# Kernel tuning notes

Measured on AMD Instinct MI355X. Metric: run time of the kernel, lower is better.

## Reference

```python
import jax, jax.numpy as jnp
import numpy as np

B, T, U, H = 4, 256, 64, 512
INNER, VOCAB = 512, 1024


def setup_inputs() -> dict:
    key = jax.random.key(0)
    ks = jax.random.split(key, 6)
    s_in = 1.0 / np.sqrt(2 * H)
    s_h = 1.0 / np.sqrt(INNER)
    return {
        "enc_state": jax.random.normal(ks[0], (B, T, H), dtype=jnp.float32),
        "dec_state": jax.random.normal(ks[1], (B, U, H), dtype=jnp.float32),
        "W1": jax.random.normal(ks[2], (2 * H, INNER), dtype=jnp.float32) * s_in,
        "b1": jnp.zeros((INNER,), dtype=jnp.float32),
        "W2": jax.random.normal(ks[3], (INNER, VOCAB), dtype=jnp.float32) * s_h,
        "b2": jnp.zeros((VOCAB,), dtype=jnp.float32),
    }


def reference(enc_state, dec_state, W1, b1, W2, b2):
    # JointNet: broadcast enc [B,T,1,H] and dec [B,1,U,H], concat -> Linear -> tanh -> Linear -> log_softmax
    # concat+Linear is split into two smaller matmuls (mathematically identical):
    # cat([e,d]) @ W1 == e @ W1[:H] + d @ W1[H:]
    enc_proj = jnp.einsum("bth,hi->bti", enc_state, W1[:H])      # [B,T,INNER]
    dec_proj = jnp.einsum("buh,hi->bui", dec_state, W1[H:])      # [B,U,INNER]
    hidden = jnp.tanh(enc_proj[:, :, None, :] + dec_proj[:, None, :, :] + b1)  # [B,T,U,INNER]
    logits = jnp.einsum("btui,iv->btuv", hidden, W2) + b2        # [B,T,U,VOCAB]
    return jax.nn.log_softmax(logits, axis=-1)
```

## Files before the change

### kernel.cpp

```cpp
#include <hip/hip_runtime.h>
#include <hip/hip_bf16.h>
#include <cstdint>
#include <cstddef>


typedef __attribute__((ext_vector_type(8))) short short8;
typedef __attribute__((ext_vector_type(4))) float f32x4;

#define BS_CHUNK 65536

#define WS_EP_OFF 0
#define WS_DP_OFF (1024 * 512 * 4)
#define WS_W2_OFF (WS_DP_OFF + 256 * 512 * 4)

#define SMEM_TOTAL (65536 + 4096 + 256 + 4096 + 256)

__device__ __forceinline__ unsigned short f2bf(float x) {
  unsigned int u = __builtin_bit_cast(unsigned int, x);
  u += 0x7FFFu + ((u >> 16) & 1u);
  return (unsigned short)(u >> 16);
}

__device__ __forceinline__ float fast_tanh(float x) {
  float ax = fabsf(x);
  float e = __expf(-2.0f * ax);
  float t = (1.0f - e) * __builtin_amdgcn_rcpf(1.0f + e);
  return copysignf(t, x);
}

__global__ __launch_bounds__(512) void prep(
    const float* __restrict__ enc, const float* __restrict__ dec,
    const float* __restrict__ W1, const float* __restrict__ b1,
    const float* __restrict__ W2,
    float* __restrict__ ep, float* __restrict__ dp, char* __restrict__ w2st) {
  __shared__ float As[8 * 512];
  const int tid = threadIdx.x;
  if (blockIdx.x < 160) {
    const int r0 = blockIdx.x * 8;
    const bool isenc = (r0 < 1024);
    const float* A = isenc ? (enc + (size_t)r0 * 512) : (dec + (size_t)(r0 - 1024) * 512);
    const float* W = isenc ? W1 : (W1 + 512 * 512);
    float* O = isenc ? (ep + (size_t)r0 * 512) : (dp + (size_t)(r0 - 1024) * 512);

    for (int idx = tid; idx < 8 * 512; idx += 512) As[idx] = A[idx];
    __syncthreads();

    const int c = tid;
    float acc[8];
#pragma unroll
    for (int r = 0; r < 8; ++r) acc[r] = 0.0f;
    const float4* As4 = (const float4*)As;
#pragma unroll 2
    for (int k4 = 0; k4 < 128; ++k4) {
      const int kb = k4 * 4;
      float w0 = W[(size_t)(kb + 0) * 512 + c];
      float w1 = W[(size_t)(kb + 1) * 512 + c];
      float w2 = W[(size_t)(kb + 2) * 512 + c];
      float w3 = W[(size_t)(kb + 3) * 512 + c];
#pragma unroll
      for (int r = 0; r < 8; ++r) {
        float4 a = As4[r * 128 + k4];
        acc[r] += a.x * w0 + a.y * w1 + a.z * w2 + a.w * w3;
      }
    }
    const float bias = isenc ? b1[c] : 0.0f;
#pragma unroll
    for (int r = 0; r < 8; ++r) O[(size_t)r * 512 + c] = acc[r] + bias;
  } else {
    const int g = (blockIdx.x - 160) * 512 + tid;
    const int v = g & 1023;
    const int kc = g >> 10;
    unsigned short vals[32];
#pragma unroll
    for (int ki = 0; ki < 32; ++ki)
      vals[ki] = f2bf(W2[(size_t)(kc * 32 + ki) * 1024 + v]);
    uint4* dst = (uint4*)(w2st + (size_t)kc * BS_CHUNK + (size_t)v * 64);
    const uint4* s = (const uint4*)vals;
    dst[0] = s[0]; dst[1] = s[1]; dst[2] = s[2]; dst[3] = s[3];
  }
}

__global__ __launch_bounds__(1024, 4) void joint(
    const float* __restrict__ ep, const float* __restrict__ dp,
    const char* __restrict__ w2st, const float* __restrict__ b2,
    float* __restrict__ out) {
  extern __shared__ char smem[];
  char* As = smem;
  float* redM = (float*)(smem + 65536);
  float* redF = redM + 1024;
  float* redS = redF + 64;
  float* redF2 = redS + 1024;

  const int tid = threadIdx.x;
  const int wave = tid >> 6, lane = tid & 63;
  const int lo = lane & 15, hi = lane >> 4;
  const int bt = blockIdx.x;
  const int m0 = bt * 64;
  const int dprow0 = (bt >> 8) * 64;
  const int nbase = wave * 64;
  const int krot = bt & 15;

  const char* bbase = w2st + (size_t)(nbase + lo) * 64 + hi * 16;

  short8 b[4];
  {
    const char* src = bbase + (size_t)krot * BS_CHUNK;
#pragma unroll
    for (int ni = 0; ni < 4; ++ni) b[ni] = *(const short8*)(src + ni * 1024);
  }

  {
    const int c0 = (tid & 63) * 8;
    const int rg = tid >> 6;
    const float* epr = ep + (size_t)bt * 512 + c0;
    float e0[8];
    *(float4*)(e0) = *(const float4*)(epr);
    *(float4*)(e0 + 4) = *(const float4*)(epr + 4);
#pragma unroll
    for (int p = 0; p < 4; ++p) {
      const int row = rg + p * 16;
      const float* dpr = dp + (size_t)(dprow0 + row) * 512 + c0;
      float d0[8];
      *(float4*)(d0) = *(const float4*)(dpr);
      *(float4*)(d0 + 4) = *(const float4*)(dpr + 4);
      unsigned short h[8];
#pragma unroll
      for (int j = 0; j < 8; ++j) h[j] = f2bf(fast_tanh(e0[j] + d0[j]));
      *(uint4*)(As + ((row * 1024 + c0 * 2) ^ ((row & 7) << 4))) = *(const uint4*)h;
    }
  }

  f32x4 acc[4][4];
#pragma unroll
  for (int mi = 0; mi < 4; ++mi)
#pragma unroll
    for (int ni = 0; ni < 4; ++ni)
#pragma unroll
      for (int j = 0; j < 4; ++j) acc[mi][ni][j] = 0.0f;

  __syncthreads();

#pragma unroll 1
  for (int kc = 0; kc < 16; ++kc) {
    int kci = kc + krot;
    kci = (kci >= 16) ? kci - 16 : kci;
    short8 bn[4];
    if (kc < 15) {
      int kn = kci + 1;
      kn = (kn >= 16) ? 0 : kn;
      const char* src = bbase + (size_t)kn * BS_CHUNK;
#pragma unroll
      for (int ni = 0; ni < 4; ++ni) bn[ni] = *(const short8*)(src + ni * 1024);
    }
    short8 a[4];
#pragma unroll
    for (int mi = 0; mi < 4; ++mi) {
      const int row = mi * 16 + lo;
      a[mi] = *(const short8*)(As + ((row * 1024 + kci * 64 + hi * 16) ^ ((row & 7) << 4)));
    }
    __builtin_amdgcn_s_setprio(1);
#pragma unroll
    for (int ni = 0; ni < 4; ++ni)
#pragma unroll
      for (int mi = 0; mi < 4; ++mi)
        acc[mi][ni] = __builtin_amdgcn_mfma_f32_16x16x32_bf16(a[mi], b[ni], acc[mi][ni], 0, 0, 0);
    __builtin_amdgcn_s_setprio(0);
    if (kc < 15) {
#pragma unroll
      for (int ni = 0; ni < 4; ++ni) b[ni] = bn[ni];
    }
  }

  float b2v[4];
#pragma unroll
  for (int ni = 0; ni < 4; ++ni) b2v[ni] = b2[nbase + ni * 16 + lo];
#pragma unroll
  for (int mi = 0; mi < 4; ++mi)
#pragma unroll
    for (int ni = 0; ni < 4; ++ni)
#pragma unroll
      for (int j = 0; j < 4; ++j) acc[mi][ni][j] += b2v[ni];

  float pm[4][4];
#pragma unroll
  for (int mi = 0; mi < 4; ++mi)
#pragma unroll
    for (int r = 0; r < 4; ++r) {
      float m = fmaxf(fmaxf(acc[mi][0][r], acc[mi][1][r]),
                      fmaxf(acc[mi][2][r], acc[mi][3][r]));
      pm[mi][r] = m;
    }
#pragma unroll
  for (int off = 1; off < 16; off <<= 1)
#pragma unroll
    for (int mi = 0; mi < 4; ++mi)
#pragma unroll
      for (int r = 0; r < 4; ++r)
        pm[mi][r] = fmaxf(pm[mi][r], __shfl_xor(pm[mi][r], off));
  if (lo == 0) {
#pragma unroll
    for (int mi = 0; mi < 4; ++mi)
#pragma unroll
      for (int r = 0; r < 4; ++r)
        redM[wave * 64 + mi * 16 + hi * 4 + r] = pm[mi][r];
  }
  __syncthreads();
  {
    const int tr = tid >> 4, w = tid & 15;
    float v = redM[w * 64 + tr];
#pragma unroll
    for (int off = 1; off < 16; off <<= 1) v = fmaxf(v, __shfl_xor(v, off));
    if (w == 0) redF[tr] = v;
  }
  __syncthreads();
  float rm[4][4];
#pragma unroll
  for (int mi = 0; mi < 4; ++mi)
#pragma unroll
    for (int r = 0; r < 4; ++r) rm[mi][r] = redF[mi * 16 + hi * 4 + r];

  float ps[4][4];
#pragma unroll
  for (int mi = 0; mi < 4; ++mi)
#pragma unroll
    for (int r = 0; r < 4; ++r) {
      float s = 0.0f;
#pragma unroll
      for (int ni = 0; ni < 4; ++ni) s += __expf(acc[mi][ni][r] - rm[mi][r]);
      ps[mi][r] = s;
    }
#pragma unroll
  for (int off = 1; off < 16; off <<= 1)
#pragma unroll
    for (int mi = 0; mi < 4; ++mi)
#pragma unroll
      for (int r = 0; r < 4; ++r)
        ps[mi][r] += __shfl_xor(ps[mi][r], off);
  if (lo == 0) {
#pragma unroll
    for (int mi = 0; mi < 4; ++mi)
#pragma unroll
      for (int r = 0; r < 4; ++r)
        redS[wave * 64 + mi * 16 + hi * 4 + r] = ps[mi][r];
  }
  __syncthreads();
  {
    const int tr = tid >> 4, w = tid & 15;
    float v = redS[w * 64 + tr];
#pragma unroll
    for (int off = 1; off < 16; off <<= 1) v += __shfl_xor(v, off);
    if (w == 0) redF2[tr] = v;
  }
  __syncthreads();

#pragma unroll
  for (int mi = 0; mi < 4; ++mi)
#pragma unroll
    for (int r = 0; r < 4; ++r) {
      const int row = mi * 16 + hi * 4 + r;
      const float sub = rm[mi][r] + __logf(redF2[row]);
      float* op = out + (size_t)(m0 + row) * 1024 + nbase + lo;
#pragma unroll
      for (int ni = 0; ni < 4; ++ni) op[ni * 16] = acc[mi][ni][r] - sub;
    }
}

extern "C" void kernel_launch(void* const* d_in, const int* in_sizes, int n_in,
                              void* d_out, int out_size, void* d_ws, size_t ws_size,
                              hipStream_t stream) {
  const float* enc = (const float*)d_in[0];
  const float* dec = (const float*)d_in[1];
  const float* W1  = (const float*)d_in[2];
  const float* b1  = (const float*)d_in[3];
  const float* W2  = (const float*)d_in[4];
  const float* b2  = (const float*)d_in[5];
  float* out = (float*)d_out;

  char* ws = (char*)d_ws;
  float* ep = (float*)(ws + WS_EP_OFF);
  float* dp = (float*)(ws + WS_DP_OFF);
  char* w2st = ws + WS_W2_OFF;

  prep<<<192, 512, 0, stream>>>(enc, dec, W1, b1, W2, ep, dp, w2st);
  joint<<<1024, 1024, SMEM_TOTAL, stream>>>(ep, dp, w2st, b2, out);
}
```

Baseline: 190.3 us.

## Make joint kernel process four row tiles per block with double-buffered W2 prefetch

The joint kernel now launches 256 blocks instead of 1024, and each block loops over four consecutive 64-row tiles. W2 fragments are kept in two register sets (P/Q) that are prefetched two K-chunks ahead, and the next tile's first chunks are loaded during the softmax epilogue. The bias load is hoisted out of the tile loop. __syncthreads is replaced by a barrier macro that only waits on LDS counters, and the setprio hints are removed. The aim is to hide global-load latency and amortise per-block setup, at the cost of fewer resident blocks per CU, so tanh/store phases may overlap less with MFMA work from other blocks.

```diff
diff --git a/kernel.cpp b/kernel.cpp
--- a/kernel.cpp
+++ b/kernel.cpp
@@ -14,6 +14,13 @@
 #define WS_W2_OFF (WS_DP_OFF + 256 * 512 * 4)
 
 #define SMEM_TOTAL (65536 + 4096 + 256 + 4096 + 256)
+
+#define BAR()                                                   \
+  do {                                                          \
+    asm volatile("s_waitcnt lgkmcnt(0)" ::: "memory");          \
+    __builtin_amdgcn_s_barrier();                               \
+    __builtin_amdgcn_sched_barrier(0);                          \
+  } while (0)
 
 __device__ __forceinline__ unsigned short f2bf(float x) {
   unsigned int u = __builtin_bit_cast(unsigned int, x);
@@ -94,175 +101,203 @@
   const int tid = threadIdx.x;
   const int wave = tid >> 6, lane = tid & 63;
   const int lo = lane & 15, hi = lane >> 4;
-  const int bt = blockIdx.x;
-  const int m0 = bt * 64;
-  const int dprow0 = (bt >> 8) * 64;
   const int nbase = wave * 64;
-  const int krot = bt & 15;
-
   const char* bbase = w2st + (size_t)(nbase + lo) * 64 + hi * 16;
 
-  short8 b[4];
+  float b2v[4];
+#pragma unroll
+  for (int ni = 0; ni < 4; ++ni) b2v[ni] = b2[nbase + ni * 16 + lo];
+
+  short8 P[4], Q[4];
   {
-    const char* src = bbase + (size_t)krot * BS_CHUNK;
-#pragma unroll
-    for (int ni = 0; ni < 4; ++ni) b[ni] = *(const short8*)(src + ni * 1024);
+    const int bt0 = blockIdx.x * 4;
+    const int kr = bt0 & 15;
+    const char* s0 = bbase + (size_t)kr * BS_CHUNK;
+    const char* s1 = bbase + (size_t)((kr + 1) & 15) * BS_CHUNK;
+#pragma unroll
+    for (int ni = 0; ni < 4; ++ni) P[ni] = *(const short8*)(s0 + ni * 1024);
+#pragma unroll
+    for (int ni = 0; ni < 4; ++ni) Q[ni] = *(const short8*)(s1 + ni * 1024);
   }
 
-  {
-    const int c0 = (tid & 63) * 8;
-    const int rg = tid >> 6;
-    const float* epr = ep + (size_t)bt * 512 + c0;
-    float e0[8];
-    *(float4*)(e0) = *(const float4*)(epr);
-    *(float4*)(e0 + 4) = *(const float4*)(epr + 4);
-#pragma unroll
-    for (int p = 0; p < 4; ++p) {
-      const int row = rg + p * 16;
-      const float* dpr = dp + (size_t)(dprow0 + row) * 512 + c0;
-      float d0[8];
-      *(float4*)(d0) = *(const float4*)(dpr);
-      *(float4*)(d0 + 4) = *(const float4*)(dpr + 4);
-      unsigned short h[8];
-#pragma unroll
-      for (int j = 0; j < 8; ++j) h[j] = f2bf(fast_tanh(e0[j] + d0[j]));
-      *(uint4*)(As + ((row * 1024 + c0 * 2) ^ ((row & 7) << 4))) = *(const uint4*)h;
-    }
+#pragma unroll 1
+  for (int t = 0; t < 4; ++t) {
+    const int bt = blockIdx.x * 4 + t;
+    const int m0 = bt * 64;
+    const int dprow0 = (bt >> 8) * 64;
+    const int krot = bt & 15;
+
+    {
+      const int c0 = (tid & 63) * 8;
+      const int rg = tid >> 6;
+      const float* epr = ep + (size_t)bt * 512 + c0;
+      float e0[8];
+      *(float4*)(e0) = *(const float4*)(epr);
+      *(float4*)(e0 + 4) = *(const float4*)(epr + 4);
+#pragma unroll
+      for (int p = 0; p < 4; ++p) {
+        const int row = rg + p * 16;
+        const float* dpr = dp + (size_t)(dprow0 + row) * 512 + c0;
+        float d0[8];
+        *(float4*)(d0) = *(const float4*)(dpr);
+        *(float4*)(d0 + 4) = *(const float4*)(dpr + 4);
+        unsigned short h[8];
+#pragma unroll
+        for (int j = 0; j < 8; ++j) h[j] = f2bf(fast_tanh(e0[j] + d0[j]));
+        *(uint4*)(As + ((row * 1024 + c0 * 2) ^ ((row & 7) << 4))) = *(const uint4*)h;
+      }
+    }
+
+    f32x4 acc[4][4];
+#pragma unroll
+    for (int mi = 0; mi < 4; ++mi)
+#pragma unroll
+      for (int ni = 0; ni < 4; ++ni)
+#pragma unroll
+        for (int j = 0; j < 4; ++j) acc[mi][ni][j] = 0.0f;
+
+    BAR();
+
+#pragma unroll 1
+    for (int i = 0; i < 8; ++i) {
+      const int c0 = (2 * i + krot) & 15;
+      const int c1 = (c0 + 1) & 15;
+      {
+        short8 a[4];
+#pragma unroll
+        for (int mi = 0; mi < 4; ++mi) {
+          const int row = mi * 16 + lo;
+          a[mi] = *(const short8*)(As + ((row * 1024 + c0 * 64 + hi * 16) ^ ((row & 7) << 4)));
+        }
+#pragma unroll
+        for (int ni = 0; ni < 4; ++ni)
+#pragma unroll
+          for (int mi = 0; mi < 4; ++mi)
+            acc[mi][ni] = __builtin_amdgcn_mfma_f32_16x16x32_bf16(a[mi], P[ni], acc[mi][ni], 0, 0, 0);
+      }
+      if (i < 7) {
+        const char* src = bbase + (size_t)((c0 + 2) & 15) * BS_CHUNK;
+#pragma unroll
+        for (int ni = 0; ni < 4; ++ni) P[ni] = *(const short8*)(src + ni * 1024);
+      }
+      {
+        short8 a[4];
+#pragma unroll
+        for (int mi = 0; mi < 4; ++mi) {
+          const int row = mi * 16 + lo;
+          a[mi] = *(const short8*)(As + ((row * 1024 + c1 * 64 + hi * 16) ^ ((row & 7) << 4)));
+        }
+#pragma unroll
+        for (int ni = 0; ni < 4; ++ni)
+#pragma unroll
+          for (int mi = 0; mi < 4; ++mi)
+            acc[mi][ni] = __builtin_amdgcn_mfma_f32_16x16x32_bf16(a[mi], Q[ni], acc[mi][ni], 0, 0, 0);
+      }
+      if (i < 7) {
+        const char* src = bbase + (size_t)((c1 + 2) & 15) * BS_CHUNK;
+#pragma unroll
+        for (int ni = 0; ni < 4; ++ni) Q[ni] = *(const short8*)(src + ni * 1024);
+      }
+    }
+
+#pragma unroll
+    for (int mi = 0; mi < 4; ++mi)
+#pragma unroll
+      for (int ni = 0; ni < 4; ++ni)
+#pragma unroll
+        for (int j = 0; j < 4; ++j) acc[mi][ni][j] += b2v[ni];
+
+    float pm[4][4];
+#pragma unroll
+    for (int mi = 0; mi < 4; ++mi)
+#pragma unroll
+      for (int r = 0; r < 4; ++r)
+        pm[mi][r] = fmaxf(fmaxf(acc[mi][0][r], acc[mi][1][r]),
+                          fmaxf(acc[mi][2][r], acc[mi][3][r]));
+#pragma unroll
+    for (int off = 1; off < 16; off <<= 1)
+#pragma unroll
+      for (int mi = 0; mi < 4; ++mi)
+#pragma unroll
+        for (int r = 0; r < 4; ++r)
+          pm[mi][r] = fmaxf(pm[mi][r], __shfl_xor(pm[mi][r], off));
+    if (lo == 0) {
+#pragma unroll
+      for (int mi = 0; mi < 4; ++mi)
+#pragma unroll
+        for (int r = 0; r < 4; ++r)
+          redM[wave * 64 + mi * 16 + hi * 4 + r] = pm[mi][r];
+    }
+    BAR();
+    {
+      const int tr = tid >> 4, w = tid & 15;
+      float v = redM[w * 64 + tr];
+#pragma unroll
+      for (int off = 1; off < 16; off <<= 1) v = fmaxf(v, __shfl_xor(v, off));
+      if (w == 0) redF[tr] = v;
+    }
+    BAR();
+    float rm[4][4];
+#pragma unroll
+    for (int mi = 0; mi < 4; ++mi)
+#pragma unroll
+      for (int r = 0; r < 4; ++r) rm[mi][r] = redF[mi * 16 + hi * 4 + r];
+
+    float ps[4][4];
+#pragma unroll
+    for (int mi = 0; mi < 4; ++mi)
+#pragma unroll
+      for (int r = 0; r < 4; ++r) {
+        float s = 0.0f;
+#pragma unroll
+        for (int ni = 0; ni < 4; ++ni) s += __expf(acc[mi][ni][r] - rm[mi][r]);
+        ps[mi][r] = s;
+      }
+#pragma unroll
+    for (int off = 1; off < 16; off <<= 1)
+#pragma unroll
+      for (int mi = 0; mi < 4; ++mi)
+#pragma unroll
+        for (int r = 0; r < 4; ++r)
+          ps[mi][r] += __shfl_xor(ps[mi][r], off);
+    if (lo == 0) {
+#pragma unroll
+      for (int mi = 0; mi < 4; ++mi)
+#pragma unroll
+        for (int r = 0; r < 4; ++r)
+          redS[wave * 64 + mi * 16 + hi * 4 + r] = ps[mi][r];
+    }
+    BAR();
+    {
+      const int tr = tid >> 4, w = tid & 15;
+      float v = redS[w * 64 + tr];
+#pragma unroll
+      for (int off = 1; off < 16; off <<= 1) v += __shfl_xor(v, off);
+      if (w == 0) redF2[tr] = v;
+    }
+    BAR();
+
+    if (t < 3) {
+      const int nrot = (bt + 1) & 15;
+      const char* s0 = bbase + (size_t)nrot * BS_CHUNK;
+      const char* s1 = bbase + (size_t)((nrot + 1) & 15) * BS_CHUNK;
+#pragma unroll
+      for (int ni = 0; ni < 4; ++ni) P[ni] = *(const short8*)(s0 + ni * 1024);
+#pragma unroll
+      for (int ni = 0; ni < 4; ++ni) Q[ni] = *(const short8*)(s1 + ni * 1024);
+    }
+
+#pragma unroll
+    for (int mi = 0; mi < 4; ++mi)
+#pragma unroll
+      for (int r = 0; r < 4; ++r) {
+        const int row = mi * 16 + hi * 4 + r;
+        const float sub = rm[mi][r] + __logf(redF2[row]);
+        float* op = out + (size_t)(m0 + row) * 1024 + nbase + lo;
+#pragma unroll
+        for (int ni = 0; ni < 4; ++ni) op[ni * 16] = acc[mi][ni][r] - sub;
+      }
   }
-
-  f32x4 acc[4][4];
-#pragma unroll
-  for (int mi = 0; mi < 4; ++mi)
-#pragma unroll
-    for (int ni = 0; ni < 4; ++ni)
-#pragma unroll
-      for (int j = 0; j < 4; ++j) acc[mi][ni][j] = 0.0f;
-
-  __syncthreads();
-
-#pragma unroll 1
-  for (int kc = 0; kc < 16; ++kc) {
-    int kci = kc + krot;
-    kci = (kci >= 16) ? kci - 16 : kci;
-    short8 bn[4];
-    if (kc < 15) {
-      int kn = kci + 1;
-      kn = (kn >= 16) ? 0 : kn;
-      const char* src = bbase + (size_t)kn * BS_CHUNK;
-#pragma unroll
-      for (int ni = 0; ni < 4; ++ni) bn[ni] = *(const short8*)(src + ni * 1024);
-    }
-    short8 a[4];
-#pragma unroll
-    for (int mi = 0; mi < 4; ++mi) {
-      const int row = mi * 16 + lo;
-      a[mi] = *(const short8*)(As + ((row * 1024 + kci * 64 + hi * 16) ^ ((row & 7) << 4)));
-    }
-    __builtin_amdgcn_s_setprio(1);
-#pragma unroll
-    for (int ni = 0; ni < 4; ++ni)
-#pragma unroll
-      for (int mi = 0; mi < 4; ++mi)
-        acc[mi][ni] = __builtin_amdgcn_mfma_f32_16x16x32_bf16(a[mi], b[ni], acc[mi][ni], 0, 0, 0);
-    __builtin_amdgcn_s_setprio(0);
-    if (kc < 15) {
-#pragma unroll
-      for (int ni = 0; ni < 4; ++ni) b[ni] = bn[ni];
-    }
-  }
-
-  float b2v[4];
-#pragma unroll
-  for (int ni = 0; ni < 4; ++ni) b2v[ni] = b2[nbase + ni * 16 + lo];
-#pragma unroll
-  for (int mi = 0; mi < 4; ++mi)
-#pragma unroll
-    for (int ni = 0; ni < 4; ++ni)
-#pragma unroll
-      for (int j = 0; j < 4; ++j) acc[mi][ni][j] += b2v[ni];
-
-  float pm[4][4];
-#pragma unroll
-  for (int mi = 0; mi < 4; ++mi)
-#pragma unroll
-    for (int r = 0; r < 4; ++r) {
-      float m = fmaxf(fmaxf(acc[mi][0][r], acc[mi][1][r]),
-                      fmaxf(acc[mi][2][r], acc[mi][3][r]));
-      pm[mi][r] = m;
-    }
-#pragma unroll
-  for (int off = 1; off < 16; off <<= 1)
-#pragma unroll
-    for (int mi = 0; mi < 4; ++mi)
-#pragma unroll
-      for (int r = 0; r < 4; ++r)
-        pm[mi][r] = fmaxf(pm[mi][r], __shfl_xor(pm[mi][r], off));
-  if (lo == 0) {
-#pragma unroll
-    for (int mi = 0; mi < 4; ++mi)
-#pragma unroll
-      for (int r = 0; r < 4; ++r)
-        redM[wave * 64 + mi * 16 + hi * 4 + r] = pm[mi][r];
-  }
-  __syncthreads();
-  {
-    const int tr = tid >> 4, w = tid & 15;
-    float v = redM[w * 64 + tr];
-#pragma unroll
-    for (int off = 1; off < 16; off <<= 1) v = fmaxf(v, __shfl_xor(v, off));
-    if (w == 0) redF[tr] = v;
-  }
-  __syncthreads();
-  float rm[4][4];
-#pragma unroll
-  for (int mi = 0; mi < 4; ++mi)
-#pragma unroll
-    for (int r = 0; r < 4; ++r) rm[mi][r] = redF[mi * 16 + hi * 4 + r];
-
-  float ps[4][4];
-#pragma unroll
-  for (int mi = 0; mi < 4; ++mi)
-#pragma unroll
-    for (int r = 0; r < 4; ++r) {
-      float s = 0.0f;
-#pragma unroll
-      for (int ni = 0; ni < 4; ++ni) s += __expf(acc[mi][ni][r] - rm[mi][r]);
-      ps[mi][r] = s;
-    }
-#pragma unroll
-  for (int off = 1; off < 16; off <<= 1)
-#pragma unroll
-    for (int mi = 0; mi < 4; ++mi)
-#pragma unroll
-      for (int r = 0; r < 4; ++r)
-        ps[mi][r] += __shfl_xor(ps[mi][r], off);
-  if (lo == 0) {
-#pragma unroll
-    for (int mi = 0; mi < 4; ++mi)
-#pragma unroll
-      for (int r = 0; r < 4; ++r)
-        redS[wave * 64 + mi * 16 + hi * 4 + r] = ps[mi][r];
-  }
-  __syncthreads();
-  {
-    const int tr = tid >> 4, w = tid & 15;
-    float v = redS[w * 64 + tr];
-#pragma unroll
-    for (int off = 1; off < 16; off <<= 1) v += __shfl_xor(v, off);
-    if (w == 0) redF2[tr] = v;
-  }
-  __syncthreads();
-
-#pragma unroll
-  for (int mi = 0; mi < 4; ++mi)
-#pragma unroll
-    for (int r = 0; r < 4; ++r) {
-      const int row = mi * 16 + hi * 4 + r;
-      const float sub = rm[mi][r] + __logf(redF2[row]);
-      float* op = out + (size_t)(m0 + row) * 1024 + nbase + lo;
-#pragma unroll
-      for (int ni = 0; ni < 4; ++ni) op[ni * 16] = acc[mi][ni][r] - sub;
-    }
 }
 
 extern "C" void kernel_launch(void* const* d_in, const int* in_sizes, int n_in,
@@ -282,5 +317,5 @@
   char* w2st = ws + WS_W2_OFF;
 
   prep<<<192, 512, 0, stream>>>(enc, dec, W1, b1, W2, ep, dp, w2st);
-  joint<<<1024, 1024, SMEM_TOTAL, stream>>>(ep, dp, w2st, b2, out);
-}
+  joint<<<256, 1024, SMEM_TOTAL, stream>>>(ep, dp, w2st, b2, out);
+}
```

Result: slower. 308.0 us (+61.9%).

## Stage W2 chunks into LDS with async double buffering and per-quarter A tiles

Applied to the files above, without the earlier changes.

The joint kernel now stages W2 K-chunks into LDS with global_load_lds, double-buffered, instead of having each wave load its B fragments straight from global memory. The tanh/bf16 activation tile is built one 128-column quarter at a time in a 16KB region, so it overlaps with the chunk loads. __syncthreads is replaced by explicit waitcnt plus s_barrier. The prep kernel's projection is split into 4-row blocks to launch more blocks. The shared-memory footprint grows to 144KB, which likely limits the kernel to one 1024-thread block per CU and trades occupancy for explicit overlap.

```diff
diff --git a/kernel.cpp b/kernel.cpp
--- a/kernel.cpp
+++ b/kernel.cpp
@@ -13,7 +13,9 @@
 #define WS_DP_OFF (1024 * 512 * 4)
 #define WS_W2_OFF (WS_DP_OFF + 256 * 512 * 4)
 
-#define SMEM_TOTAL (65536 + 4096 + 256 + 4096 + 256)
+#define LDS_B0 16384
+#define LDS_B1 81920
+#define SMEM_TOTAL 147456
 
 __device__ __forceinline__ unsigned short f2bf(float x) {
   unsigned int u = __builtin_bit_cast(unsigned int, x);
@@ -33,24 +35,22 @@
     const float* __restrict__ W1, const float* __restrict__ b1,
     const float* __restrict__ W2,
     float* __restrict__ ep, float* __restrict__ dp, char* __restrict__ w2st) {
-  __shared__ float As[8 * 512];
+  __shared__ float As[4 * 512];
   const int tid = threadIdx.x;
-  if (blockIdx.x < 160) {
-    const int r0 = blockIdx.x * 8;
+  if (blockIdx.x < 320) {
+    const int r0 = blockIdx.x * 4;
     const bool isenc = (r0 < 1024);
     const float* A = isenc ? (enc + (size_t)r0 * 512) : (dec + (size_t)(r0 - 1024) * 512);
     const float* W = isenc ? W1 : (W1 + 512 * 512);
     float* O = isenc ? (ep + (size_t)r0 * 512) : (dp + (size_t)(r0 - 1024) * 512);
 
-    for (int idx = tid; idx < 8 * 512; idx += 512) As[idx] = A[idx];
+    for (int idx = tid; idx < 4 * 512; idx += 512) As[idx] = A[idx];
     __syncthreads();
 
     const int c = tid;
-    float acc[8];
-#pragma unroll
-    for (int r = 0; r < 8; ++r) acc[r] = 0.0f;
+    float acc[4] = {0.f, 0.f, 0.f, 0.f};
     const float4* As4 = (const float4*)As;
-#pragma unroll 2
+#pragma unroll 4
     for (int k4 = 0; k4 < 128; ++k4) {
       const int kb = k4 * 4;
       float w0 = W[(size_t)(kb + 0) * 512 + c];
@@ -58,16 +58,16 @@
       float w2 = W[(size_t)(kb + 2) * 512 + c];
       float w3 = W[(size_t)(kb + 3) * 512 + c];
 #pragma unroll
-      for (int r = 0; r < 8; ++r) {
+      for (int r = 0; r < 4; ++r) {
         float4 a = As4[r * 128 + k4];
         acc[r] += a.x * w0 + a.y * w1 + a.z * w2 + a.w * w3;
       }
     }
     const float bias = isenc ? b1[c] : 0.0f;
 #pragma unroll
-    for (int r = 0; r < 8; ++r) O[(size_t)r * 512 + c] = acc[r] + bias;
+    for (int r = 0; r < 4; ++r) O[(size_t)r * 512 + c] = acc[r] + bias;
   } else {
-    const int g = (blockIdx.x - 160) * 512 + tid;
+    const int g = (blockIdx.x - 320) * 512 + tid;
     const int v = g & 1023;
     const int kc = g >> 10;
     unsigned short vals[32];
@@ -80,13 +80,24 @@
   }
 }
 
+__device__ __forceinline__ void stage_chunk(const char* __restrict__ w2st,
+                                            char* dstbuf, int gc, int wave, int lane) {
+  const char* src = w2st + (size_t)gc * BS_CHUNK + wave * 4096 + (size_t)lane * 16;
+  char* dst = dstbuf + wave * 4096 + lane * 16;
+#pragma unroll
+  for (int jj = 0; jj < 4; ++jj)
+    __builtin_amdgcn_global_load_lds(
+        (const __attribute__((address_space(1))) unsigned int*)(src + jj * 1024),
+        (__attribute__((address_space(3))) unsigned int*)(dst + jj * 1024), 16, 0, 0);
+}
+
 __global__ __launch_bounds__(1024, 4) void joint(
     const float* __restrict__ ep, const float* __restrict__ dp,
     const char* __restrict__ w2st, const float* __restrict__ b2,
     float* __restrict__ out) {
   extern __shared__ char smem[];
-  char* As = smem;
-  float* redM = (float*)(smem + 65536);
+  char* Asm = smem;
+  float* redM = (float*)smem;
   float* redF = redM + 1024;
   float* redS = redF + 64;
   float* redF2 = redS + 1024;
@@ -98,98 +109,109 @@
   const int m0 = bt * 64;
   const int dprow0 = (bt >> 8) * 64;
   const int nbase = wave * 64;
-  const int krot = bt & 15;
-
-  const char* bbase = w2st + (size_t)(nbase + lo) * 64 + hi * 16;
-
-  short8 b[4];
+  const int krot4 = bt & 3;
+
+  const int tr = tid >> 4;
+  const int tc = (tid & 15) * 8;
+
+  float b2v[4];
+#pragma unroll
+  for (int ni = 0; ni < 4; ++ni) b2v[ni] = b2[nbase + ni * 16 + lo];
+
+  float e0[8], d0[8];
   {
-    const char* src = bbase + (size_t)krot * BS_CHUNK;
-#pragma unroll
-    for (int ni = 0; ni < 4; ++ni) b[ni] = *(const short8*)(src + ni * 1024);
-  }
-
+    const float* epr = ep + (size_t)bt * 512 + tc;
+    *(float4*)(e0) = ((const float4*)epr)[0];
+    *(float4*)(e0 + 4) = ((const float4*)epr)[1];
+    const float* dpr = dp + (size_t)(dprow0 + tr) * 512 + tc;
+    *(float4*)(d0) = ((const float4*)dpr)[0];
+    *(float4*)(d0 + 4) = ((const float4*)dpr)[1];
+  }
+  stage_chunk(w2st, smem + LDS_B0, (0 + krot4) & 3, wave, lane);
+  stage_chunk(w2st, smem + LDS_B1, (1 + krot4) & 3, wave, lane);
+  __builtin_amdgcn_sched_barrier(0);
   {
-    const int c0 = (tid & 63) * 8;
-    const int rg = tid >> 6;
-    const float* epr = ep + (size_t)bt * 512 + c0;
-    float e0[8];
-    *(float4*)(e0) = *(const float4*)(epr);
-    *(float4*)(e0 + 4) = *(const float4*)(epr + 4);
-#pragma unroll
-    for (int p = 0; p < 4; ++p) {
-      const int row = rg + p * 16;
-      const float* dpr = dp + (size_t)(dprow0 + row) * 512 + c0;
-      float d0[8];
-      *(float4*)(d0) = *(const float4*)(dpr);
-      *(float4*)(d0 + 4) = *(const float4*)(dpr + 4);
+    unsigned short h[8];
+#pragma unroll
+    for (int j = 0; j < 8; ++j) h[j] = f2bf(fast_tanh(e0[j] + d0[j]));
+    *(uint4*)(Asm + ((tr * 256 + tc * 2) ^ ((tr & 7) << 4))) = *(const uint4*)h;
+  }
+
+  f32x4 acc[4][4];
+#pragma unroll
+  for (int mi = 0; mi < 4; ++mi)
+#pragma unroll
+    for (int ni = 0; ni < 4; ++ni)
+#pragma unroll
+      for (int j = 0; j < 4; ++j) acc[mi][ni][j] = 0.0f;
+
+#pragma unroll
+  for (int q = 0; q < 4; ++q) {
+    if (q) {
+      const float* epr = ep + (size_t)bt * 512 + q * 128 + tc;
+      float e1[8], d1[8];
+      *(float4*)(e1) = ((const float4*)epr)[0];
+      *(float4*)(e1 + 4) = ((const float4*)epr)[1];
+      const float* dpr = dp + (size_t)(dprow0 + tr) * 512 + q * 128 + tc;
+      *(float4*)(d1) = ((const float4*)dpr)[0];
+      *(float4*)(d1 + 4) = ((const float4*)dpr)[1];
       unsigned short h[8];
 #pragma unroll
-      for (int j = 0; j < 8; ++j) h[j] = f2bf(fast_tanh(e0[j] + d0[j]));
-      *(uint4*)(As + ((row * 1024 + c0 * 2) ^ ((row & 7) << 4))) = *(const uint4*)h;
-    }
-  }
-
-  f32x4 acc[4][4];
+      for (int j = 0; j < 8; ++j) h[j] = f2bf(fast_tanh(e1[j] + d1[j]));
+      *(uint4*)(Asm + ((tr * 256 + tc * 2) ^ ((tr & 7) << 4))) = *(const uint4*)h;
+    }
+#pragma unroll
+    for (int ii = 0; ii < 4; ++ii) {
+      const int i = q * 4 + ii;
+      if (i == 15) asm volatile("s_waitcnt vmcnt(0) lgkmcnt(0)" ::: "memory");
+      else         asm volatile("s_waitcnt vmcnt(4) lgkmcnt(0)" ::: "memory");
+      __builtin_amdgcn_s_barrier();
+      __builtin_amdgcn_sched_barrier(0);
+
+      char* rdbuf = smem + ((i & 1) ? LDS_B1 : LDS_B0);
+      const int cif = (i + krot4) & 3;
+      short8 bfr[4], afr[4];
+      const char* bp = rdbuf + (size_t)(nbase + lo) * 64 + hi * 16;
+#pragma unroll
+      for (int ni = 0; ni < 4; ++ni) bfr[ni] = *(const short8*)(bp + ni * 1024);
+#pragma unroll
+      for (int mi = 0; mi < 4; ++mi) {
+        const int row = mi * 16 + lo;
+        afr[mi] = *(const short8*)(Asm + ((row * 256 + cif * 64 + hi * 16) ^ ((row & 7) << 4)));
+      }
+      asm volatile("s_waitcnt lgkmcnt(0)" ::: "memory");
+      __builtin_amdgcn_sched_barrier(0);
+      __builtin_amdgcn_s_barrier();
+      __builtin_amdgcn_sched_barrier(0);
+
+      if (i < 14) {
+        const int j = i + 2;
+        const int gc = (j >> 2) * 4 + ((j + krot4) & 3);
+        stage_chunk(w2st, rdbuf, gc, wave, lane);
+        __builtin_amdgcn_sched_barrier(0);
+      }
+#pragma unroll
+      for (int ni = 0; ni < 4; ++ni)
+#pragma unroll
+        for (int mi = 0; mi < 4; ++mi)
+          acc[mi][ni] = __builtin_amdgcn_mfma_f32_16x16x32_bf16(afr[mi], bfr[ni], acc[mi][ni], 0, 0, 0);
+    }
+  }
+
 #pragma unroll
   for (int mi = 0; mi < 4; ++mi)
 #pragma unroll
     for (int ni = 0; ni < 4; ++ni)
 #pragma unroll
-      for (int j = 0; j < 4; ++j) acc[mi][ni][j] = 0.0f;
-
-  __syncthreads();
-
-#pragma unroll 1
-  for (int kc = 0; kc < 16; ++kc) {
-    int kci = kc + krot;
-    kci = (kci >= 16) ? kci - 16 : kci;
-    short8 bn[4];
-    if (kc < 15) {
-      int kn = kci + 1;
-      kn = (kn >= 16) ? 0 : kn;
-      const char* src = bbase + (size_t)kn * BS_CHUNK;
-#pragma unroll
-      for (int ni = 0; ni < 4; ++ni) bn[ni] = *(const short8*)(src + ni * 1024);
-    }
-    short8 a[4];
-#pragma unroll
-    for (int mi = 0; mi < 4; ++mi) {
-      const int row = mi * 16 + lo;
-      a[mi] = *(const short8*)(As + ((row * 1024 + kci * 64 + hi * 16) ^ ((row & 7) << 4)));
-    }
-    __builtin_amdgcn_s_setprio(1);
-#pragma unroll
-    for (int ni = 0; ni < 4; ++ni)
-#pragma unroll
-      for (int mi = 0; mi < 4; ++mi)
-        acc[mi][ni] = __builtin_amdgcn_mfma_f32_16x16x32_bf16(a[mi], b[ni], acc[mi][ni], 0, 0, 0);
-    __builtin_amdgcn_s_setprio(0);
-    if (kc < 15) {
-#pragma unroll
-      for (int ni = 0; ni < 4; ++ni) b[ni] = bn[ni];
-    }
-  }
-
-  float b2v[4];
-#pragma unroll
-  for (int ni = 0; ni < 4; ++ni) b2v[ni] = b2[nbase + ni * 16 + lo];
-#pragma unroll
-  for (int mi = 0; mi < 4; ++mi)
-#pragma unroll
-    for (int ni = 0; ni < 4; ++ni)
-#pragma unroll
       for (int j = 0; j < 4; ++j) acc[mi][ni][j] += b2v[ni];
 
   float pm[4][4];
 #pragma unroll
   for (int mi = 0; mi < 4; ++mi)
 #pragma unroll
-    for (int r = 0; r < 4; ++r) {
-      float m = fmaxf(fmaxf(acc[mi][0][r], acc[mi][1][r]),
-                      fmaxf(acc[mi][2][r], acc[mi][3][r]));
-      pm[mi][r] = m;
-    }
+    for (int r = 0; r < 4; ++r)
+      pm[mi][r] = fmaxf(fmaxf(acc[mi][0][r], acc[mi][1][r]),
+                        fmaxf(acc[mi][2][r], acc[mi][3][r]));
 #pragma unroll
   for (int off = 1; off < 16; off <<= 1)
 #pragma unroll
@@ -204,15 +226,17 @@
       for (int r = 0; r < 4; ++r)
         redM[wave * 64 + mi * 16 + hi * 4 + r] = pm[mi][r];
   }
-  __syncthreads();
+  asm volatile("s_waitcnt lgkmcnt(0)" ::: "memory");
+  __builtin_amdgcn_s_barrier();
   {
-    const int tr = tid >> 4, w = tid & 15;
-    float v = redM[w * 64 + tr];
+    const int rr = tid >> 4, w = tid & 15;
+    float v = redM[w * 64 + rr];
 #pragma unroll
     for (int off = 1; off < 16; off <<= 1) v = fmaxf(v, __shfl_xor(v, off));
-    if (w == 0) redF[tr] = v;
-  }
-  __syncthreads();
+    if (w == 0) redF[rr] = v;
+  }
+  asm volatile("s_waitcnt lgkmcnt(0)" ::: "memory");
+  __builtin_amdgcn_s_barrier();
   float rm[4][4];
 #pragma unroll
   for (int mi = 0; mi < 4; ++mi)
@@ -243,15 +267,17 @@
       for (int r = 0; r < 4; ++r)
         redS[wave * 64 + mi * 16 + hi * 4 + r] = ps[mi][r];
   }
-  __syncthreads();
+  asm volatile("s_waitcnt lgkmcnt(0)" ::: "memory");
+  __builtin_amdgcn_s_barrier();
   {
-    const int tr = tid >> 4, w = tid & 15;
-    float v = redS[w * 64 + tr];
+    const int rr = tid >> 4, w = tid & 15;
+    float v = redS[w * 64 + rr];
 #pragma unroll
     for (int off = 1; off < 16; off <<= 1) v += __shfl_xor(v, off);
-    if (w == 0) redF2[tr] = v;
-  }
-  __syncthreads();
+    if (w == 0) redF2[rr] = v;
+  }
+  asm volatile("s_waitcnt lgkmcnt(0)" ::: "memory");
+  __builtin_amdgcn_s_barrier();
 
 #pragma unroll
   for (int mi = 0; mi < 4; ++mi)
@@ -281,6 +307,6 @@
   float* dp = (float*)(ws + WS_DP_OFF);
   char* w2st = ws + WS_W2_OFF;
 
-  prep<<<192, 512, 0, stream>>>(enc, dec, W1, b1, W2, ep, dp, w2st);
+  prep<<<352, 512, 0, stream>>>(enc, dec, W1, b1, W2, ep, dp, w2st);
   joint<<<1024, 1024, SMEM_TOTAL, stream>>>(ep, dp, w2st, b2, out);
 }
```

New measurement: 257.5 us. 35.3% more time.

## Split joint kernel into tiled GEMM with fp16 logits plus separate log-softmax pass

Applied to the files above, without the earlier changes.

Replaces the fused GEMM+log_softmax kernel with two kernels. The first is a 256x256-tiled GEMM that recomputes tanh(enc+dec) per k-chunk into double-buffered LDS and writes bias-added logits as fp16 into the output buffer. The second is a per-row log-softmax kernel that reads those fp16 values back and overwrites the row in place with fp32 results. The intent is to free the GEMM from the block-wide softmax reductions and their barriers. In exchange it adds an extra write and read of the full logits, repeats the tanh work across the four N blocks, rounds logits to fp16, and drops the max subtraction, which risks overflow and accuracy loss.

```diff
diff --git a/kernel.cpp b/kernel.cpp
--- a/kernel.cpp
+++ b/kernel.cpp
@@ -13,12 +13,19 @@
 #define WS_DP_OFF (1024 * 512 * 4)
 #define WS_W2_OFF (WS_DP_OFF + 256 * 512 * 4)
 
-#define SMEM_TOTAL (65536 + 4096 + 256 + 4096 + 256)
-
 __device__ __forceinline__ unsigned short f2bf(float x) {
   unsigned int u = __builtin_bit_cast(unsigned int, x);
   u += 0x7FFFu + ((u >> 16) & 1u);
   return (unsigned short)(u >> 16);
+}
+
+__device__ __forceinline__ unsigned short f2h(float x) {
+  _Float16 h = (_Float16)x;
+  return __builtin_bit_cast(unsigned short, h);
+}
+
+__device__ __forceinline__ float h2f(unsigned short u) {
+  return (float)__builtin_bit_cast(_Float16, u);
 }
 
 __device__ __forceinline__ float fast_tanh(float x) {
@@ -80,54 +87,41 @@
   }
 }
 
-__global__ __launch_bounds__(1024, 4) void joint(
+__global__ __launch_bounds__(1024, 4) void joint_gemm(
     const float* __restrict__ ep, const float* __restrict__ dp,
     const char* __restrict__ w2st, const float* __restrict__ b2,
     float* __restrict__ out) {
-  extern __shared__ char smem[];
-  char* As = smem;
-  float* redM = (float*)(smem + 65536);
-  float* redF = redM + 1024;
-  float* redS = redF + 64;
-  float* redF2 = redS + 1024;
+  __shared__ char As[2][256 * 64];
 
   const int tid = threadIdx.x;
   const int wave = tid >> 6, lane = tid & 63;
   const int lo = lane & 15, hi = lane >> 4;
-  const int bt = blockIdx.x;
-  const int m0 = bt * 64;
-  const int dprow0 = (bt >> 8) * 64;
-  const int nbase = wave * 64;
-  const int krot = bt & 15;
+  const int wm = wave >> 2, wn = wave & 3;
+  const int m = blockIdx.x & 255, n = blockIdx.x >> 8;
+  const int row0 = m * 256;
+  const int nbase = n * 256 + wn * 64;
+
+  const int tr = tid >> 2;
+  const int ts = tid & 3;
+  const int grow = row0 + tr;
+  const int gbt = grow >> 6;
+  const int gdr = ((gbt >> 8) << 6) + (grow & 63);
+  const float* eprow = ep + (size_t)gbt * 512 + ts * 8;
+  const float* dprow = dp + (size_t)gdr * 512 + ts * 8;
+  const int wofs = tr * 64 + ((ts ^ ((tr >> 1) & 3)) << 4);
 
   const char* bbase = w2st + (size_t)(nbase + lo) * 64 + hi * 16;
 
-  short8 b[4];
   {
-    const char* src = bbase + (size_t)krot * BS_CHUNK;
-#pragma unroll
-    for (int ni = 0; ni < 4; ++ni) b[ni] = *(const short8*)(src + ni * 1024);
-  }
-
-  {
-    const int c0 = (tid & 63) * 8;
-    const int rg = tid >> 6;
-    const float* epr = ep + (size_t)bt * 512 + c0;
-    float e0[8];
-    *(float4*)(e0) = *(const float4*)(epr);
-    *(float4*)(e0 + 4) = *(const float4*)(epr + 4);
-#pragma unroll
-    for (int p = 0; p < 4; ++p) {
-      const int row = rg + p * 16;
-      const float* dpr = dp + (size_t)(dprow0 + row) * 512 + c0;
-      float d0[8];
-      *(float4*)(d0) = *(const float4*)(dpr);
-      *(float4*)(d0 + 4) = *(const float4*)(dpr + 4);
-      unsigned short h[8];
-#pragma unroll
-      for (int j = 0; j < 8; ++j) h[j] = f2bf(fast_tanh(e0[j] + d0[j]));
-      *(uint4*)(As + ((row * 1024 + c0 * 2) ^ ((row & 7) << 4))) = *(const uint4*)h;
-    }
+    float e[8], d[8];
+    *(float4*)(e) = *(const float4*)(eprow);
+    *(float4*)(e + 4) = *(const float4*)(eprow + 4);
+    *(float4*)(d) = *(const float4*)(dprow);
+    *(float4*)(d + 4) = *(const float4*)(dprow + 4);
+    unsigned short h[8];
+#pragma unroll
+    for (int j = 0; j < 8; ++j) h[j] = f2bf(fast_tanh(e[j] + d[j]));
+    *(uint4*)(As[0] + wofs) = *(const uint4*)h;
   }
 
   f32x4 acc[4][4];
@@ -142,127 +136,86 @@
 
 #pragma unroll 1
   for (int kc = 0; kc < 16; ++kc) {
-    int kci = kc + krot;
-    kci = (kci >= 16) ? kci - 16 : kci;
-    short8 bn[4];
+    short8 b[4];
+    const char* bp = bbase + (size_t)kc * BS_CHUNK;
+#pragma unroll
+    for (int ni = 0; ni < 4; ++ni) b[ni] = *(const short8*)(bp + ni * 1024);
+
     if (kc < 15) {
-      int kn = kci + 1;
-      kn = (kn >= 16) ? 0 : kn;
-      const char* src = bbase + (size_t)kn * BS_CHUNK;
-#pragma unroll
-      for (int ni = 0; ni < 4; ++ni) bn[ni] = *(const short8*)(src + ni * 1024);
-    }
+      float e[8], d[8];
+      const float* e_ = eprow + (kc + 1) * 32;
+      const float* d_ = dprow + (kc + 1) * 32;
+      *(float4*)(e) = *(const float4*)(e_);
+      *(float4*)(e + 4) = *(const float4*)(e_ + 4);
+      *(float4*)(d) = *(const float4*)(d_);
+      *(float4*)(d + 4) = *(const float4*)(d_ + 4);
+      unsigned short h[8];
+#pragma unroll
+      for (int j = 0; j < 8; ++j) h[j] = f2bf(fast_tanh(e[j] + d[j]));
+      *(uint4*)(As[(kc + 1) & 1] + wofs) = *(const uint4*)h;
+    }
+
     short8 a[4];
 #pragma unroll
     for (int mi = 0; mi < 4; ++mi) {
-      const int row = mi * 16 + lo;
-      a[mi] = *(const short8*)(As + ((row * 1024 + kci * 64 + hi * 16) ^ ((row & 7) << 4)));
-    }
-    __builtin_amdgcn_s_setprio(1);
+      const int r = wm * 64 + mi * 16 + lo;
+      a[mi] = *(const short8*)(As[kc & 1] + r * 64 + ((hi ^ ((r >> 1) & 3)) << 4));
+    }
 #pragma unroll
     for (int ni = 0; ni < 4; ++ni)
 #pragma unroll
       for (int mi = 0; mi < 4; ++mi)
         acc[mi][ni] = __builtin_amdgcn_mfma_f32_16x16x32_bf16(a[mi], b[ni], acc[mi][ni], 0, 0, 0);
-    __builtin_amdgcn_s_setprio(0);
-    if (kc < 15) {
-#pragma unroll
-      for (int ni = 0; ni < 4; ++ni) b[ni] = bn[ni];
-    }
+
+    __syncthreads();
   }
 
   float b2v[4];
 #pragma unroll
   for (int ni = 0; ni < 4; ++ni) b2v[ni] = b2[nbase + ni * 16 + lo];
+
+  unsigned short* outh = (unsigned short*)out;
 #pragma unroll
   for (int mi = 0; mi < 4; ++mi)
 #pragma unroll
-    for (int ni = 0; ni < 4; ++ni)
-#pragma unroll
-      for (int j = 0; j < 4; ++j) acc[mi][ni][j] += b2v[ni];
-
-  float pm[4][4];
-#pragma unroll
-  for (int mi = 0; mi < 4; ++mi)
-#pragma unroll
     for (int r = 0; r < 4; ++r) {
-      float m = fmaxf(fmaxf(acc[mi][0][r], acc[mi][1][r]),
-                      fmaxf(acc[mi][2][r], acc[mi][3][r]));
-      pm[mi][r] = m;
-    }
-#pragma unroll
-  for (int off = 1; off < 16; off <<= 1)
-#pragma unroll
-    for (int mi = 0; mi < 4; ++mi)
-#pragma unroll
-      for (int r = 0; r < 4; ++r)
-        pm[mi][r] = fmaxf(pm[mi][r], __shfl_xor(pm[mi][r], off));
-  if (lo == 0) {
-#pragma unroll
-    for (int mi = 0; mi < 4; ++mi)
-#pragma unroll
-      for (int r = 0; r < 4; ++r)
-        redM[wave * 64 + mi * 16 + hi * 4 + r] = pm[mi][r];
-  }
-  __syncthreads();
-  {
-    const int tr = tid >> 4, w = tid & 15;
-    float v = redM[w * 64 + tr];
-#pragma unroll
-    for (int off = 1; off < 16; off <<= 1) v = fmaxf(v, __shfl_xor(v, off));
-    if (w == 0) redF[tr] = v;
-  }
-  __syncthreads();
-  float rm[4][4];
-#pragma unroll
-  for (int mi = 0; mi < 4; ++mi)
-#pragma unroll
-    for (int r = 0; r < 4; ++r) rm[mi][r] = redF[mi * 16 + hi * 4 + r];
-
-  float ps[4][4];
-#pragma unroll
-  for (int mi = 0; mi < 4; ++mi)
-#pragma unroll
-    for (int r = 0; r < 4; ++r) {
-      float s = 0.0f;
-#pragma unroll
-      for (int ni = 0; ni < 4; ++ni) s += __expf(acc[mi][ni][r] - rm[mi][r]);
-      ps[mi][r] = s;
-    }
-#pragma unroll
-  for (int off = 1; off < 16; off <<= 1)
-#pragma unroll
-    for (int mi = 0; mi < 4; ++mi)
-#pragma unroll
-      for (int r = 0; r < 4; ++r)
-        ps[mi][r] += __shfl_xor(ps[mi][r], off);
-  if (lo == 0) {
-#pragma unroll
-    for (int mi = 0; mi < 4; ++mi)
-#pragma unroll
-      for (int r = 0; r < 4; ++r)
-        redS[wave * 64 + mi * 16 + hi * 4 + r] = ps[mi][r];
-  }
-  __syncthreads();
-  {
-    const int tr = tid >> 4, w = tid & 15;
-    float v = redS[w * 64 + tr];
-#pragma unroll
-    for (int off = 1; off < 16; off <<= 1) v += __shfl_xor(v, off);
-    if (w == 0) redF2[tr] = v;
-  }
-  __syncthreads();
-
-#pragma unroll
-  for (int mi = 0; mi < 4; ++mi)
-#pragma unroll
-    for (int r = 0; r < 4; ++r) {
-      const int row = mi * 16 + hi * 4 + r;
-      const float sub = rm[mi][r] + __logf(redF2[row]);
-      float* op = out + (size_t)(m0 + row) * 1024 + nbase + lo;
-#pragma unroll
-      for (int ni = 0; ni < 4; ++ni) op[ni * 16] = acc[mi][ni][r] - sub;
-    }
+      const int row = row0 + wm * 64 + mi * 16 + hi * 4 + r;
+      unsigned short* op = outh + (size_t)row * 2048 + nbase + lo;
+#pragma unroll
+      for (int ni = 0; ni < 4; ++ni)
+        op[ni * 16] = f2h(acc[mi][ni][r] + b2v[ni]);
+    }
+}
+
+__global__ __launch_bounds__(256) void lsm(float* __restrict__ out) {
+  const int gw = (blockIdx.x * 256 + threadIdx.x) >> 6;
+  const int lane = threadIdx.x & 63;
+#pragma unroll 1
+  for (int r = gw; r < 65536; r += 8192) {
+    const unsigned short* lp = (const unsigned short*)out + (size_t)r * 2048 + lane * 16;
+    uint4 q0 = *(const uint4*)(lp);
+    uint4 q1 = *(const uint4*)(lp + 8);
+    unsigned short us[16];
+    *(uint4*)(us) = q0;
+    *(uint4*)(us + 8) = q1;
+    float v[16];
+#pragma unroll
+    for (int j = 0; j < 16; ++j) v[j] = h2f(us[j]);
+    float s = 0.0f;
+#pragma unroll
+    for (int j = 0; j < 16; ++j) s += __expf(v[j]);
+#pragma unroll
+    for (int off = 1; off < 64; off <<= 1) s += __shfl_xor(s, off);
+    const float ls = __logf(s);
+    float o[16];
+#pragma unroll
+    for (int j = 0; j < 16; ++j) o[j] = v[j] - ls;
+    float* op = out + (size_t)r * 1024 + lane * 16;
+    *(float4*)(op) = *(const float4*)(o);
+    *(float4*)(op + 4) = *(const float4*)(o + 4);
+    *(float4*)(op + 8) = *(const float4*)(o + 8);
+    *(float4*)(op + 12) = *(const float4*)(o + 12);
+  }
 }
 
 extern "C" void kernel_launch(void* const* d_in, const int* in_sizes, int n_in,
@@ -282,5 +235,6 @@
   char* w2st = ws + WS_W2_OFF;
 
   prep<<<192, 512, 0, stream>>>(enc, dec, W1, b1, W2, ep, dp, w2st);
-  joint<<<1024, 1024, SMEM_TOTAL, stream>>>(ep, dp, w2st, b2, out);
-}
+  joint_gemm<<<1024, 1024, 0, stream>>>(ep, dp, w2st, b2, out);
+  lsm<<<2048, 256, 0, stream>>>(out);
+}
```

Measured after the change: 271.9 us. 1.43x slower.
